# Kernel tuning notes

Hardware: AMD Instinct MI355X
Metric: run time of the kernel (lower is better)

## Reference

```python
import jax, jax.numpy as jnp
import numpy as np


def haar_dwt2(x):
    """Single-level 2D Haar DWT on last two axes, matching pywt.dwt2('haar').

    x: [..., H, W] with H, W even.
    Returns [..., 4, H/2, W/2] stacked as (LL, LH, HL, HH) where, per pywt,
    LH=cH (highpass along H, lowpass along W), HL=cV, HH=cD.
    """
    B, C, H, W = x.shape
    # group 2x2 blocks: [B, C, H/2, 2, W/2, 2]
    xb = x.reshape(B, C, H // 2, 2, W // 2, 2)
    x00 = xb[:, :, :, 0, :, 0]  # even row, even col
    x01 = xb[:, :, :, 0, :, 1]  # even row, odd col
    x10 = xb[:, :, :, 1, :, 0]  # odd row, even col
    x11 = xb[:, :, :, 1, :, 1]  # odd row, odd col
    half = jnp.asarray(0.5, dtype=x.dtype)
    LL = (x00 + x01 + x10 + x11) * half
    LH = (x00 + x01 - x10 - x11) * half  # cH: detail along rows (H)
    HL = (x00 - x01 + x10 - x11) * half  # cV: detail along cols (W)
    HH = (x00 - x01 - x10 + x11) * half  # cD: detail both axes
    return jnp.stack([LL, LH, HL, HH], axis=1)  # [B, 4, C, H/2, W/2]


def setup_inputs() -> dict:
    key = jax.random.key(0)
    x = jax.random.normal(key, (8, 32, 512, 512), dtype=jnp.float32)
    return {"input": x}


def reference(input):
    return haar_dwt2(input)
```

## Files before the change

### kernel.cpp

```cpp
#include <hip/hip_runtime.h>


#define B_   8
#define C_   32
#define H2_  256
#define W2_  256
#define WQ_  (W2_/4)

typedef float v4f __attribute__((ext_vector_type(4)));

__global__ __launch_bounds__(256)
void WaveletTransform_14319420965150_kernel(const float* __restrict__ x,
                                            float* __restrict__ out) {
    const int total  = B_ * C_ * H2_ * WQ_;
    const int stride = gridDim.x * blockDim.x;

    const v4f* __restrict__ xin = (const v4f*)x;
    v4f* __restrict__ o         = (v4f*)out;
    const size_t qstride = (size_t)C_ * (H2_ * W2_ / 4);

    for (int tid = blockIdx.x * blockDim.x + threadIdx.x; tid < total; tid += stride) {
        const int wq = tid & (WQ_ - 1);
        const int h2 = (tid >> 6) & (H2_ - 1);
        const int bc = tid >> 14;

        const size_t r0 = ((size_t)bc * 512 + 2 * h2) * (512 / 4) + 2 * wq;
        v4f t0 = xin[r0];
        v4f t1 = xin[r0 + 1];
        v4f u0 = xin[r0 + 128];
        v4f u1 = xin[r0 + 129];

        v4f LL, LH, HL, HH;
        { float s0 = t0.x + t0.y, d0 = t0.x - t0.y;
          float s1 = u0.x + u0.y, d1 = u0.x - u0.y;
          LL.x = (s0 + s1) * 0.5f; LH.x = (s0 - s1) * 0.5f;
          HL.x = (d0 + d1) * 0.5f; HH.x = (d0 - d1) * 0.5f; }
        { float s0 = t0.z + t0.w, d0 = t0.z - t0.w;
          float s1 = u0.z + u0.w, d1 = u0.z - u0.w;
          LL.y = (s0 + s1) * 0.5f; LH.y = (s0 - s1) * 0.5f;
          HL.y = (d0 + d1) * 0.5f; HH.y = (d0 - d1) * 0.5f; }
        { float s0 = t1.x + t1.y, d0 = t1.x - t1.y;
          float s1 = u1.x + u1.y, d1 = u1.x - u1.y;
          LL.z = (s0 + s1) * 0.5f; LH.z = (s0 - s1) * 0.5f;
          HL.z = (d0 + d1) * 0.5f; HH.z = (d0 - d1) * 0.5f; }
        { float s0 = t1.z + t1.w, d0 = t1.z - t1.w;
          float s1 = u1.z + u1.w, d1 = u1.z - u1.w;
          LL.w = (s0 + s1) * 0.5f; LH.w = (s0 - s1) * 0.5f;
          HL.w = (d0 + d1) * 0.5f; HH.w = (d0 - d1) * 0.5f; }

        const size_t ob = ((size_t)(bc >> 5) * (4 * C_) + (bc & (C_ - 1))) * (H2_ * W2_ / 4)
                        + (size_t)h2 * (W2_ / 4) + wq;
        o[ob]               = LL;
        o[ob +     qstride] = LH;
        o[ob + 2 * qstride] = HL;
        o[ob + 3 * qstride] = HH;
    }
}

extern "C" void kernel_launch(void* const* d_in, const int* in_sizes, int n_in,
                              void* d_out, int out_size, void* d_ws, size_t ws_size,
                              hipStream_t stream) {
    const float* x = (const float*)d_in[0];
    float* out = (float*)d_out;
    const int block = 256;
    const int grid  = 2048;
    WaveletTransform_14319420965150_kernel<<<grid, block, 0, stream>>>(x, out);
}
```

Baseline: 434.9 us.

## Stage row sums/differences in LDS so each wave writes one output subband

Replaces the grid-stride loop with one block per 16-row tile. Each thread loads rows, computes horizontal sums and differences, and stores them in shared memory. After a barrier, each wave writes one contiguous subband (LL/LH/HL/HH) for 8 output rows. The aim is fewer scattered store streams per wave and more loads in flight per thread, at the cost of LDS traffic and a barrier.

```diff
diff --git a/kernel.cpp b/kernel.cpp
--- a/kernel.cpp
+++ b/kernel.cpp
@@ -1,59 +1,58 @@
 #include <hip/hip_runtime.h>
 
 
-#define B_   8
-#define C_   32
-#define H2_  256
-#define W2_  256
-#define WQ_  (W2_/4)
-
+#define C_ 32
 typedef float v4f __attribute__((ext_vector_type(4)));
 
 __global__ __launch_bounds__(256)
 void WaveletTransform_14319420965150_kernel(const float* __restrict__ x,
                                             float* __restrict__ out) {
-    const int total  = B_ * C_ * H2_ * WQ_;
-    const int stride = gridDim.x * blockDim.x;
+    __shared__ v4f sd[2][16][64];
+
+    const int bid = blockIdx.x;
+    const int bc  = bid >> 5;
+    const int h2b = bid & 31;
 
     const v4f* __restrict__ xin = (const v4f*)x;
     v4f* __restrict__ o         = (v4f*)out;
-    const size_t qstride = (size_t)C_ * (H2_ * W2_ / 4);
 
-    for (int tid = blockIdx.x * blockDim.x + threadIdx.x; tid < total; tid += stride) {
-        const int wq = tid & (WQ_ - 1);
-        const int h2 = (tid >> 6) & (H2_ - 1);
-        const int bc = tid >> 14;
+    const int t    = threadIdx.x;
+    const int lane = t & 63;
+    const int wid  = t >> 6;
 
-        const size_t r0 = ((size_t)bc * 512 + 2 * h2) * (512 / 4) + 2 * wq;
-        v4f t0 = xin[r0];
-        v4f t1 = xin[r0 + 1];
-        v4f u0 = xin[r0 + 128];
-        v4f u1 = xin[r0 + 129];
+    const size_t imgbase = (size_t)bc * 65536 + (size_t)h2b * (16 * 128);
 
-        v4f LL, LH, HL, HH;
-        { float s0 = t0.x + t0.y, d0 = t0.x - t0.y;
-          float s1 = u0.x + u0.y, d1 = u0.x - u0.y;
-          LL.x = (s0 + s1) * 0.5f; LH.x = (s0 - s1) * 0.5f;
-          HL.x = (d0 + d1) * 0.5f; HH.x = (d0 - d1) * 0.5f; }
-        { float s0 = t0.z + t0.w, d0 = t0.z - t0.w;
-          float s1 = u0.z + u0.w, d1 = u0.z - u0.w;
-          LL.y = (s0 + s1) * 0.5f; LH.y = (s0 - s1) * 0.5f;
-          HL.y = (d0 + d1) * 0.5f; HH.y = (d0 - d1) * 0.5f; }
-        { float s0 = t1.x + t1.y, d0 = t1.x - t1.y;
-          float s1 = u1.x + u1.y, d1 = u1.x - u1.y;
-          LL.z = (s0 + s1) * 0.5f; LH.z = (s0 - s1) * 0.5f;
-          HL.z = (d0 + d1) * 0.5f; HH.z = (d0 - d1) * 0.5f; }
-        { float s0 = t1.z + t1.w, d0 = t1.z - t1.w;
-          float s1 = u1.z + u1.w, d1 = u1.z - u1.w;
-          LL.w = (s0 + s1) * 0.5f; LH.w = (s0 - s1) * 0.5f;
-          HL.w = (d0 + d1) * 0.5f; HH.w = (d0 - d1) * 0.5f; }
+    v4f a[4], b[4];
+    #pragma unroll
+    for (int j = 0; j < 4; ++j) {
+        const size_t g = imgbase + (size_t)(4 * j + wid) * 128 + 2 * lane;
+        a[j] = xin[g];
+        b[j] = xin[g + 1];
+    }
+    #pragma unroll
+    for (int j = 0; j < 4; ++j) {
+        const int r = 4 * j + wid;
+        v4f s = { a[j].x + a[j].y, a[j].z + a[j].w,
+                  b[j].x + b[j].y, b[j].z + b[j].w };
+        v4f d = { a[j].x - a[j].y, a[j].z - a[j].w,
+                  b[j].x - b[j].y, b[j].z - b[j].w };
+        sd[0][r][lane] = s;
+        sd[1][r][lane] = d;
+    }
+    __syncthreads();
 
-        const size_t ob = ((size_t)(bc >> 5) * (4 * C_) + (bc & (C_ - 1))) * (H2_ * W2_ / 4)
-                        + (size_t)h2 * (W2_ / 4) + wq;
-        o[ob]               = LL;
-        o[ob +     qstride] = LH;
-        o[ob + 2 * qstride] = HL;
-        o[ob + 3 * qstride] = HH;
+    const int q = wid;
+    const int p = q >> 1;
+    const bool neg = (q & 1);
+    size_t ob = ((size_t)(bc >> 5) * 128 + (size_t)q * C_ + (bc & (C_ - 1))) * 16384
+              + (size_t)(h2b * 8) * 64 + lane;
+
+    #pragma unroll
+    for (int r = 0; r < 8; ++r) {
+        v4f top = sd[p][2 * r][lane];
+        v4f bot = sd[p][2 * r + 1][lane];
+        v4f res = neg ? (top - bot) * 0.5f : (top + bot) * 0.5f;
+        o[ob + (size_t)r * 64] = res;
     }
 }
 
@@ -63,6 +62,6 @@
     const float* x = (const float*)d_in[0];
     float* out = (float*)d_out;
     const int block = 256;
-    const int grid  = 2048;
+    const int grid  = 8192;
     WaveletTransform_14319420965150_kernel<<<grid, block, 0, stream>>>(x, out);
 }
```

New measurement: 426.1 us. -2.0%, faster.
